# Performance work log

Measured on AMD Instinct MI355X. Metric: run time of the kernel, lower is better.

The kernel has to match this reference:

```python
import jax, jax.numpy as jnp
import numpy as np
from jax import lax

B, N, K = 4, 4096, 64
M1, M2 = 2048, 410  # fps ratios 0.5 then 0.2 (ceil)
EPS = 1e-5  # BatchNorm1d eps


def bn_eval(h, g, be):
    # BatchNorm1d in eval mode with init running stats (mean=0, var=1)
    return h * (g / jnp.sqrt(1.0 + EPS)) + be


def mlp(x, params):
    # Seq(Lin, ReLU, BN) per layer
    for (W, b, g, be) in params:
        x = bn_eval(jax.nn.relu(x @ W + b), g, be)
    return x


def fps(pos, m):
    # farthest point sampling on pos [n,3]; deterministic start at index 0
    n = pos.shape[0]

    def step(carry, _):
        dists, last = carry
        d = jnp.sum((pos - pos[last]) ** 2, axis=-1)
        dists = jnp.minimum(dists, d)
        nxt = jnp.argmax(dists).astype(jnp.int32)
        return (dists, nxt), nxt

    _, rest = lax.scan(step, (jnp.full((n,), jnp.inf, pos.dtype), jnp.int32(0)), None, length=m - 1)
    return jnp.concatenate([jnp.zeros((1,), jnp.int32), rest])


def ball_query(src, q, r):
    # up to K nearest neighbors of each query within radius r
    d2 = jnp.sum((q[:, None, :] - src[None, :, :]) ** 2, axis=-1)  # [M,N]
    negd, idx = lax.top_k(-d2, K)
    return idx, (-negd) <= r * r


def point_conv(x, src_pos, q_pos, idx, mask, params):
    # PyG PointConv: msg = nn(cat[x_j, pos_j - pos_i]); max aggregation
    xj = x[idx]                              # [M,K,C]
    rel = src_pos[idx] - q_pos[:, None, :]   # [M,K,3]
    h = mlp(jnp.concatenate([xj, rel], axis=-1), params)  # [M,K,F]
    h = jnp.where(mask[:, :, None], h, -jnp.inf)
    out = jnp.max(h, axis=1)
    return jnp.where(jnp.any(mask, axis=1)[:, None], out, 0.0)


def sa_module(x, pos, m, radii, params):
    # x [B,n,C], pos [B,n,3]
    idx = jax.vmap(lambda p: fps(p, m))(pos)                       # [B,m]
    q_pos = jnp.take_along_axis(pos, idx[:, :, None], axis=1)      # [B,m,3]
    outs = []
    for r in radii:
        nidx, mask = jax.vmap(lambda s, q: ball_query(s, q, r))(pos, q_pos)
        out = jax.vmap(lambda a, sp, qp, ni, mk: point_conv(a, sp, qp, ni, mk, params))(x, pos, q_pos, nidx, mask)
        outs.append(out)
    return jnp.concatenate(outs, axis=-1), q_pos


def forward(xyz, color, p1, p2, p3, wl1, bl1, wl2, bl2):
    x1, pos1 = sa_module(color, xyz, M1, (0.2, 0.1), p1)     # [B,M1,128]
    x2, pos2 = sa_module(x1, pos1, M2, (0.35, 0.5), p2)      # [B,M2,512]
    h = mlp(jnp.concatenate([x2, pos2], axis=-1), p3)        # [B,M2,1024]
    g = jnp.max(h, axis=1)                                   # global max pool -> [B,1024]
    h1 = jax.nn.relu(g @ wl1 + bl1)                          # dropout inactive (eval)
    out = h1 @ wl2 + bl2
    return out / jnp.linalg.norm(out, axis=1, keepdims=True)


def setup_inputs():
    key = jax.random.key(0)
    ks = jax.random.split(key, 10)

    def w(k, shape):
        return jax.random.normal(k, shape, jnp.float32) * 0.05

    z = lambda n: jnp.zeros((n,), jnp.float32)
    o = lambda n: jnp.ones((n,), jnp.float32)
    return dict(
        xyz=jax.random.uniform(ks[0], (B, N, 3), jnp.float32),
        color=jax.random.uniform(ks[1], (B, N, 3), jnp.float32),
        w1a=w(ks[2], (6, 64)), b1a=z(64), g1a=o(64), be1a=z(64),
        w1b=w(ks[3], (64, 64)), b1b=z(64), g1b=o(64), be1b=z(64),
        w2a=w(ks[4], (131, 128)), b2a=z(128), g2a=o(128), be2a=z(128),
        w2b=w(ks[5], (128, 256)), b2b=z(256), g2b=o(256), be2b=z(256),
        w3=w(ks[6], (515, 1024)), b3=z(1024), g3=o(1024), be3=z(1024),
        wl1=w(ks[7], (1024, 512)), bl1=z(512),
        wl2=w(ks[8], (512, 128)), bl2=z(128),
    )


def reference(xyz, color, w1a, b1a, g1a, be1a, w1b, b1b, g1b, be1b,
              w2a, b2a, g2a, be2a, w2b, b2b, g2b, be2b,
              w3, b3, g3, be3, wl1, bl1, wl2, bl2):
    p1 = [(w1a, b1a, g1a, be1a), (w1b, b1b, g1b, be1b)]
    p2 = [(w2a, b2a, g2a, be2a), (w2b, b2b, g2b, be2b)]
    p3 = [(w3, b3, g3, be3)]
    return forward(xyz, color, p1, p2, p3, wl1, bl1, wl2, bl2)
```

## Files before the change

kernel.cpp:

```cpp
#include <hip/hip_runtime.h>
#include <stdint.h>

#define DEV __device__ __forceinline__

DEV float d2_exact(float ax, float ay, float az, float bx, float by, float bz) {
    float dx = __fsub_rn(ax, bx);
    float dy = __fsub_rn(ay, by);
    float dz = __fsub_rn(az, bz);
    return __fadd_rn(__fadd_rn(__fmul_rn(dx, dx), __fmul_rn(dy, dy)), __fmul_rn(dz, dz));
}

DEV void atomicMaxF(float* a, float v) {
    if (v >= 0.f) atomicMax((int*)a, __float_as_int(v));
    else          atomicMin((unsigned int*)a, __float_as_uint(v));
}

DEV void wave_lds_sync() {
    asm volatile("s_waitcnt lgkmcnt(0)" ::: "memory");
    __builtin_amdgcn_wave_barrier();
}

template<bool MAXRED>
DEV unsigned long long wave_red_u64_l63(unsigned long long k) {
    unsigned lo = (unsigned)k, hi = (unsigned)(k >> 32);
#define DPP_RED_STEP(ctrl, rmask)                                                          \
    {                                                                                      \
        unsigned nlo = (unsigned)__builtin_amdgcn_update_dpp((int)lo, (int)lo, ctrl,       \
                                                             rmask, 0xF, false);           \
        unsigned nhi = (unsigned)__builtin_amdgcn_update_dpp((int)hi, (int)hi, ctrl,       \
                                                             rmask, 0xF, false);           \
        unsigned long long cur = ((unsigned long long)hi << 32) | lo;                      \
        unsigned long long oth = ((unsigned long long)nhi << 32) | nlo;                    \
        bool take = MAXRED ? (oth > cur) : (oth < cur);                                    \
        lo = take ? nlo : lo;                                                              \
        hi = take ? nhi : hi;                                                              \
    }
    DPP_RED_STEP(0x111, 0xF)
    DPP_RED_STEP(0x112, 0xF)
    DPP_RED_STEP(0x114, 0xF)
    DPP_RED_STEP(0x118, 0xF)
    DPP_RED_STEP(0x142, 0xA)
    DPP_RED_STEP(0x143, 0xC)
#undef DPP_RED_STEP
    return ((unsigned long long)hi << 32) | lo;
}

DEV unsigned long long bcast_l63(unsigned long long k) {
    unsigned lo = (unsigned)__builtin_amdgcn_readlane((int)(unsigned)k, 63);
    unsigned hi = (unsigned)__builtin_amdgcn_readlane((int)(unsigned)(k >> 32), 63);
    return ((unsigned long long)hi << 32) | lo;
}

DEV int wave_incl_scan_i32(int v) {
    int t;
    t = __builtin_amdgcn_update_dpp(0, v, 0x111, 0xF, 0xF, true);  v += t;
    t = __builtin_amdgcn_update_dpp(0, v, 0x112, 0xF, 0xF, true);  v += t;
    t = __builtin_amdgcn_update_dpp(0, v, 0x114, 0xF, 0xF, true);  v += t;
    t = __builtin_amdgcn_update_dpp(0, v, 0x118, 0xF, 0xF, true);  v += t;
    t = __builtin_amdgcn_update_dpp(0, v, 0x142, 0xA, 0xF, false); v += t;
    t = __builtin_amdgcn_update_dpp(0, v, 0x143, 0xC, 0xF, false); v += t;
    return v;
}

DEV unsigned wave_min_u32_bcast(unsigned v) {
    int x = (int)v, t;
#define MINSTEP(ctrl, rmask)                                              \
    t = __builtin_amdgcn_update_dpp(-1, x, ctrl, rmask, 0xF, false);      \
    x = ((unsigned)t < (unsigned)x) ? t : x;
    MINSTEP(0x111, 0xF) MINSTEP(0x112, 0xF) MINSTEP(0x114, 0xF)
    MINSTEP(0x118, 0xF) MINSTEP(0x142, 0xA) MINSTEP(0x143, 0xC)
#undef MINSTEP
    return (unsigned)__builtin_amdgcn_readlane(x, 63);
}

DEV void topk64_radix(const float* __restrict__ cD, const int* __restrict__ cI,
                      int cnt, int* buckets, int* nbr, int lane) {
    unsigned prefix = 0;
    int need = 64;
    int shift;
    int done_le_shift = -1;
    for (shift = 24; shift >= 0; shift -= 8) {
        for (int i = lane; i < 256; i += 64) buckets[i] = 0;
        wave_lds_sync();
        for (int e = lane; e < cnt; e += 64) {
            unsigned db = __float_as_uint(cD[e]);
            bool match = (shift == 24) || ((db >> (shift + 8)) == prefix);
            if (match) atomicAdd(&buckets[(db >> shift) & 255], 1);
        }
        wave_lds_sync();
        int c0 = buckets[4 * lane + 0], c1 = buckets[4 * lane + 1];
        int c2 = buckets[4 * lane + 2], c3 = buckets[4 * lane + 3];
        int lsum = c0 + c1 + c2 + c3;
        int excl = wave_incl_scan_i32(lsum) - lsum;
        unsigned packed = 0xFFFFFFFFu;
        int cum = excl;
        int cc[4] = {c0, c1, c2, c3};
#pragma unroll
        for (int j = 0; j < 4; j++) {
            if (cum < need && need <= cum + cc[j])
                packed = ((unsigned)(4 * lane + j) << 20) | (unsigned)cum;
            cum += cc[j];
        }
        unsigned win = wave_min_u32_bcast(packed);
        int B = (int)(win >> 20);
        int bef = (int)(win & 0xFFFFF);
        need -= bef;
        prefix = (shift == 24) ? (unsigned)B : ((prefix << 8) | (unsigned)B);
        int cntB = buckets[B];
        if (cntB == need) { done_le_shift = shift; break; }
    }
    int base = 0;
    if (done_le_shift >= 0) {
        int s = done_le_shift;
        unsigned Pv = prefix;
        for (int e0 = 0; e0 < cnt; e0 += 64) {
            int e = e0 + lane;
            bool sel = false;
            if (e < cnt) sel = ((__float_as_uint(cD[e]) >> s) <= Pv);
            unsigned long long mk = __ballot(sel);
            int pre = __popcll(mk & ((1ull << lane) - 1ull));
            if (sel) nbr[base + pre] = cI[e];
            base += __popcll(mk);
        }
    } else {
        unsigned T = prefix;
        for (int e0 = 0; e0 < cnt; e0 += 64) {
            int e = e0 + lane;
            bool sel = false;
            if (e < cnt) sel = (__float_as_uint(cD[e]) < T);
            unsigned long long mk = __ballot(sel);
            int pre = __popcll(mk & ((1ull << lane) - 1ull));
            if (sel) nbr[base + pre] = cI[e];
            base += __popcll(mk);
        }
        int lastIdx = -1;
        for (int k = 0; k < need; k++) {
            unsigned best = 0xFFFFFFFFu;
            for (int e = lane; e < cnt; e += 64) {
                if (__float_as_uint(cD[e]) == T) {
                    int ix = cI[e];
                    if (ix > lastIdx && (unsigned)ix < best) best = (unsigned)ix;
                }
            }
            best = wave_min_u32_bcast(best);
            if (lane == 0) nbr[base + k] = (int)best;
            lastIdx = (int)best;
        }
    }
}

template<int N, int M, int TPB>
DEV void fps_body(const float* __restrict__ P, float* __restrict__ Q,
                  float* sP, unsigned long long* skey) {
    constexpr int PPT = N / TPB;
    constexpr int NW = TPB / 64;
    const int tid = threadIdx.x;
    const int w = tid >> 6;
    const int lane = tid & 63;

    for (int e = tid; e < N * 3; e += TPB) sP[e] = P[e];
    __syncthreads();

    float px[PPT], py[PPT], pz[PPT], mind[PPT];
#pragma unroll
    for (int p = 0; p < PPT; p++) {
        int i = tid + p * TPB;
        px[p] = sP[3 * i]; py[p] = sP[3 * i + 1]; pz[p] = sP[3 * i + 2];
        mind[p] = __builtin_inff();
    }
    float cx = sP[0], cy = sP[1], cz = sP[2];
    if (tid == 0) { Q[0] = cx; Q[1] = cy; Q[2] = cz; }

    for (int s = 1; s < M; s++) {
        float bestm = -1.f;
        int bidx = 0;
#pragma unroll
        for (int p = 0; p < PPT; p++) {
            float d = d2_exact(px[p], py[p], pz[p], cx, cy, cz);
            float m = fminf(mind[p], d);
            mind[p] = m;
            if (m > bestm) { bestm = m; bidx = tid + p * TPB; }
        }
        unsigned long long key =
            ((unsigned long long)__float_as_uint(bestm) << 32) | (unsigned)(0x7FFFFFFF - bidx);
        key = wave_red_u64_l63<true>(key);
        if (lane == 63) skey[(s & 1) * NW + w] = key;
        __syncthreads();
        const ulonglong2* kv = (const ulonglong2*)(skey + (s & 1) * NW);
        unsigned long long kk = 0ull;
#pragma unroll
        for (int i = 0; i < NW / 2; i++) {
            ulonglong2 v = kv[i];
            unsigned long long m2 = (v.x > v.y) ? v.x : v.y;
            kk = (m2 > kk) ? m2 : kk;
        }
        int sel = 0x7FFFFFFF - (int)(unsigned)(kk & 0xFFFFFFFFu);
        cx = sP[3 * sel]; cy = sP[3 * sel + 1]; cz = sP[3 * sel + 2];
        if (tid == 0) { Q[3 * s] = cx; Q[3 * s + 1] = cy; Q[3 * s + 2] = cz; }
    }
}

__global__ __launch_bounds__(256)
void fps1_kernel(const float* __restrict__ pos, float* __restrict__ qpos) {
    __shared__ float sP[4096 * 3];
    __shared__ __align__(16) unsigned long long skey[2 * 4];
    const int b = blockIdx.x;
    fps_body<4096, 2048, 256>(pos + (size_t)b * 4096 * 3, qpos + (size_t)b * 2048 * 3, sP, skey);
}

#define SA1_CAP 1024

struct Sa1Lds {
    float candD[4][SA1_CAP];
    int   candI[4][SA1_CAP];
    int   nbrS[4][64];
    int   buckets[4][256];
    float vbuf[4][64][8];
    float h1buf[4][64];
};
struct Fps2Lds {
    float sP[2048 * 3];
    unsigned long long skey[2 * 4];
};
union Sa1FusedLds { Sa1Lds sa; Fps2Lds fps; };

__global__ __launch_bounds__(256)
void sa1_fps2_kernel(const float* __restrict__ pos, const float* __restrict__ color,
                     const float* __restrict__ qpos1, float* __restrict__ qpos2,
                     const float* __restrict__ w1, const float* __restrict__ b1,
                     const float* __restrict__ g1, const float* __restrict__ be1,
                     const float* __restrict__ w2, const float* __restrict__ b2,
                     const float* __restrict__ g2, const float* __restrict__ be2,
                     float* __restrict__ x1) {
    __shared__ __align__(16) Sa1FusedLds u;

    if (blockIdx.x < 4) {
        const int b = blockIdx.x;
        fps_body<2048, 410, 256>(qpos1 + (size_t)b * 2048 * 3, qpos2 + (size_t)b * 410 * 3,
                                 u.fps.sP, u.fps.skey);
        return;
    }

    const int lane = threadIdx.x & 63;
    const int w = threadIdx.x >> 6;

    float w1c[6];
#pragma unroll
    for (int i = 0; i < 6; i++) w1c[i] = w1[i * 64 + lane];
    float w2c[64];
#pragma unroll
    for (int i = 0; i < 64; i++) w2c[i] = w2[i * 64 + lane];
    const float rs = rsqrtf(1.0f + 1e-5f);
    const float b1f = b1[lane], s1f = g1[lane] * rs, be1f = be1[lane];
    const float b2f = b2[lane], s2f = g2[lane] * rs, be2f = be2[lane];

    const int gw = (blockIdx.x - 4) * 4 + w;

    for (int it = 0; it < 8; ++it) {
        int p = gw * 8 + it;
        int b = p >> 12;
        int rad = (p >> 11) & 1;
        int q = p & 2047;
        float r2 = (rad == 0) ? (float)(0.2 * 0.2) : (float)(0.1 * 0.1);
        const float* P = pos + (size_t)b * 4096 * 3;
        const float* C = color + (size_t)b * 4096 * 3;
        const float* QP = qpos1 + ((size_t)b * 2048 + q) * 3;
        float qx = QP[0], qy = QP[1], qz = QP[2];

        int cnt = 0;
        for (int c0 = 0; c0 < 4096; c0 += 64) {
            int j = c0 + lane;
            float d2 = d2_exact(P[3 * j], P[3 * j + 1], P[3 * j + 2], qx, qy, qz);
            bool pr = (d2 <= r2);
            unsigned long long mk = __ballot(pr);
            int pre = __popcll(mk & ((1ull << lane) - 1ull));
            int dst = cnt + pre;
            if (pr && dst < SA1_CAP) { u.sa.candD[w][dst] = d2; u.sa.candI[w][dst] = j; }
            cnt += __popcll(mk);
        }
        wave_lds_sync();

        int nV;
        if (cnt <= 64) {
            nV = cnt;
            if (lane < cnt) u.sa.nbrS[w][lane] = u.sa.candI[w][lane];
        } else {
            nV = 64;
            if (cnt <= SA1_CAP) {
                topk64_radix(u.sa.candD[w], u.sa.candI[w], cnt,
                             u.sa.buckets[w], u.sa.nbrS[w], lane);
            } else {
                unsigned long long lastK = 0ull;
                for (int k = 0; k < 64; k++) {
                    unsigned long long bk = ~0ull;
                    for (int j = lane; j < 4096; j += 64) {
                        float d2 = d2_exact(P[3 * j], P[3 * j + 1], P[3 * j + 2], qx, qy, qz);
                        if (d2 <= r2) {
                            unsigned long long ke =
                                ((unsigned long long)__float_as_uint(d2) << 32) | (unsigned)(j + 1);
                            if (ke > lastK && ke < bk) bk = ke;
                        }
                    }
                    bk = wave_red_u64_l63<false>(bk);
                    bk = bcast_l63(bk);
                    if (lane == 0) u.sa.nbrS[w][k] = (int)(unsigned)(bk & 0xFFFFFFFFu) - 1;
                    lastK = bk;
                }
            }
        }
        wave_lds_sync();

        if (lane < nV) {
            int j = u.sa.nbrS[w][lane];
            u.sa.vbuf[w][lane][0] = C[3 * j];
            u.sa.vbuf[w][lane][1] = C[3 * j + 1];
            u.sa.vbuf[w][lane][2] = C[3 * j + 2];
            u.sa.vbuf[w][lane][3] = P[3 * j] - qx;
            u.sa.vbuf[w][lane][4] = P[3 * j + 1] - qy;
            u.sa.vbuf[w][lane][5] = P[3 * j + 2] - qz;
        }
        wave_lds_sync();

        float m = -__builtin_inff();
        for (int n = 0; n < nV; n++) {
            float4 v0 = *reinterpret_cast<const float4*>(&u.sa.vbuf[w][n][0]);
            float4 v1 = *reinterpret_cast<const float4*>(&u.sa.vbuf[w][n][4]);
            float h = b1f;
            h = fmaf(v0.x, w1c[0], h); h = fmaf(v0.y, w1c[1], h); h = fmaf(v0.z, w1c[2], h);
            h = fmaf(v0.w, w1c[3], h); h = fmaf(v1.x, w1c[4], h); h = fmaf(v1.y, w1c[5], h);
            h = fmaxf(h, 0.f);
            h = fmaf(h, s1f, be1f);
            u.sa.h1buf[w][lane] = h;
            wave_lds_sync();
            float a = b2f;
#pragma unroll
            for (int i4 = 0; i4 < 16; i4++) {
                float4 hv = *reinterpret_cast<const float4*>(&u.sa.h1buf[w][i4 * 4]);
                a = fmaf(hv.x, w2c[4 * i4 + 0], a);
                a = fmaf(hv.y, w2c[4 * i4 + 1], a);
                a = fmaf(hv.z, w2c[4 * i4 + 2], a);
                a = fmaf(hv.w, w2c[4 * i4 + 3], a);
            }
            a = fmaxf(a, 0.f);
            a = fmaf(a, s2f, be2f);
            m = fmaxf(m, a);
            __builtin_amdgcn_wave_barrier();
        }
        x1[((size_t)b * 2048 + q) * 128 + rad * 64 + lane] = (nV > 0) ? m : 0.f;
    }
}

struct S2Lds {
    float cD[4][2048];
    int   cI[4][2048];
    int   buckets[4][256];
};
struct YpreLds { float xr[4][4][128]; };
union S2FusedLds { S2Lds s2; YpreLds yp; };

__global__ __launch_bounds__(256)
void sa2sel_ypre_kernel(const float* __restrict__ qpos1, const float* __restrict__ qpos2,
                        int* __restrict__ cntOut, int* __restrict__ nbrOut,
                        const float* __restrict__ x1, const float* __restrict__ w2a,
                        const float* __restrict__ b2a, float* __restrict__ y) {
    __shared__ __align__(16) S2FusedLds u;
    const int lane = threadIdx.x & 63;
    const int w = threadIdx.x >> 6;

    if (blockIdx.x >= 820) {
        int r0 = ((blockIdx.x - 820) * 4 + w) * 4;
#pragma unroll
        for (int rr = 0; rr < 4; rr++) {
            const float* X = x1 + (size_t)(r0 + rr) * 128;
            u.yp.xr[w][rr][lane] = X[lane];
            u.yp.xr[w][rr][lane + 64] = X[lane + 64];
        }
        wave_lds_sync();
        float acc[4][2];
#pragma unroll
        for (int rr = 0; rr < 4; rr++) { acc[rr][0] = b2a[lane]; acc[rr][1] = b2a[lane + 64]; }
        for (int i = 0; i < 128; i++) {
            float w0 = w2a[i * 128 + lane];
            float w1v = w2a[i * 128 + 64 + lane];
#pragma unroll
            for (int rr = 0; rr < 4; rr++) {
                float xv = u.yp.xr[w][rr][i];
                acc[rr][0] = fmaf(xv, w0, acc[rr][0]);
                acc[rr][1] = fmaf(xv, w1v, acc[rr][1]);
            }
        }
#pragma unroll
        for (int rr = 0; rr < 4; rr++) {
            y[(size_t)(r0 + rr) * 128 + lane] = acc[rr][0];
            y[(size_t)(r0 + rr) * 128 + 64 + lane] = acc[rr][1];
        }
        return;
    }

    int p = blockIdx.x * 4 + w;
    int rad = p & 1;
    int q = (p >> 1) % 410;
    int b = (p >> 1) / 410;
    float r2 = (rad == 0) ? (float)(0.35 * 0.35) : 0.25f;
    const float* S = qpos1 + (size_t)b * 2048 * 3;
    const float* QP = qpos2 + ((size_t)b * 410 + q) * 3;
    float qx = QP[0], qy = QP[1], qz = QP[2];

    int cnt = 0;
    for (int c0 = 0; c0 < 2048; c0 += 64) {
        int j = c0 + lane;
        float d2 = d2_exact(S[3 * j], S[3 * j + 1], S[3 * j + 2], qx, qy, qz);
        bool pr = (d2 <= r2);
        unsigned long long mk = __ballot(pr);
        int pre = __popcll(mk & ((1ull << lane) - 1ull));
        if (pr) { u.s2.cD[w][cnt + pre] = d2; u.s2.cI[w][cnt + pre] = j; }
        cnt += __popcll(mk);
    }
    wave_lds_sync();

    int nV = (cnt < 64) ? cnt : 64;
    if (cnt <= 64) {
        if (lane < cnt) nbrOut[(size_t)p * 64 + lane] = u.s2.cI[w][lane];
    } else {
        topk64_radix(u.s2.cD[w], u.s2.cI[w], cnt,
                     u.s2.buckets[w], nbrOut + (size_t)p * 64, lane);
    }
    if (lane == 0) cntOut[p] = nV;
}

__global__ __launch_bounds__(256)
void sa2gemm_kernel(const float* __restrict__ y, const float* __restrict__ qpos1,
                    const float* __restrict__ qpos2, const float* __restrict__ w2a,
                    const float* __restrict__ g2a, const float* __restrict__ be2a,
                    const float* __restrict__ w2b, const float* __restrict__ b2b,
                    const float* __restrict__ g2b, const float* __restrict__ be2b,
                    const int* __restrict__ cntIn, const int* __restrict__ nbrIn,
                    float* __restrict__ A3) {
    __shared__ __align__(16) float h1T[128][68];
    __shared__ __align__(16) float Bs[16][256];
    __shared__ int nbrS[64];

    const int tid = threadIdx.x;
    const int lane = tid & 63;
    const int w = tid >> 6;
    int p = blockIdx.x;
    int rad = p & 1;
    int q = (p >> 1) % 410;
    int b = (p >> 1) / 410;
    int nV = cntIn[p];
    if (tid < 64) nbrS[tid] = nbrIn[(size_t)p * 64 + tid];
    __syncthreads();

    const float* QP = qpos2 + ((size_t)b * 410 + q) * 3;
    float qx = QP[0], qy = QP[1], qz = QP[2];
    const float rs = rsqrtf(1.0f + 1e-5f);
    float wr0a = w2a[128 * 128 + lane], wr1a = w2a[129 * 128 + lane], wr2a = w2a[130 * 128 + lane];
    float wr0b = w2a[128 * 128 + 64 + lane], wr1b = w2a[129 * 128 + 64 + lane], wr2b = w2a[130 * 128 + 64 + lane];
    float sA = g2a[lane] * rs, beA = be2a[lane];
    float sB = g2a[64 + lane] * rs, beB = be2a[64 + lane];

    for (int n = w; n < 64; n += 4) {
        float v0 = 0.f, v1 = 0.f;
        if (n < nV) {
            int j = nbrS[n];
            const float* Y = y + ((size_t)b * 2048 + j) * 128;
            const float* S = qpos1 + ((size_t)b * 2048 + j) * 3;
            float rx = S[0] - qx, ry = S[1] - qy, rz = S[2] - qz;
            float p0 = Y[lane];
            p0 = fmaf(rx, wr0a, p0); p0 = fmaf(ry, wr1a, p0); p0 = fmaf(rz, wr2a, p0);
            float p1 = Y[64 + lane];
            p1 = fmaf(rx, wr0b, p1); p1 = fmaf(ry, wr1b, p1); p1 = fmaf(rz, wr2b, p1);
            v0 = fmaf(fmaxf(p0, 0.f), sA, beA);
            v1 = fmaf(fmaxf(p1, 0.f), sB, beB);
        }
        h1T[lane][n] = v0;
        h1T[64 + lane][n] = v1;
    }
    __syncthreads();

    const int tn = tid & 7;
    const int tf = tid >> 3;
    float acc[8][8];
#pragma unroll
    for (int r = 0; r < 8; r++)
#pragma unroll
        for (int c = 0; c < 8; c++) acc[r][c] = 0.f;

    for (int kt = 0; kt < 8; kt++) {
        __syncthreads();
#pragma unroll
        for (int i = 0; i < 16; i++) {
            int ee = tid + 256 * i;
            int r = ee >> 8, c = ee & 255;
            Bs[r][c] = w2b[(kt * 16 + r) * 256 + c];
        }
        __syncthreads();
#pragma unroll
        for (int kk = 0; kk < 16; kk++) {
            float4 a0 = *reinterpret_cast<const float4*>(&h1T[kt * 16 + kk][tn * 8]);
            float4 a1 = *reinterpret_cast<const float4*>(&h1T[kt * 16 + kk][tn * 8 + 4]);
            float4 b0 = *reinterpret_cast<const float4*>(&Bs[kk][tf * 8]);
            float4 b1 = *reinterpret_cast<const float4*>(&Bs[kk][tf * 8 + 4]);
            float av[8] = {a0.x, a0.y, a0.z, a0.w, a1.x, a1.y, a1.z, a1.w};
            float bv[8] = {b0.x, b0.y, b0.z, b0.w, b1.x, b1.y, b1.z, b1.w};
#pragma unroll
            for (int r = 0; r < 8; r++)
#pragma unroll
                for (int c = 0; c < 8; c++) acc[r][c] = fmaf(av[r], bv[c], acc[r][c]);
        }
    }

    const int f2 = tf * 8;
    float bb[8], ss[8], beb[8];
#pragma unroll
    for (int c = 0; c < 8; c++) {
        bb[c] = b2b[f2 + c];
        ss[c] = g2b[f2 + c] * rs;
        beb[c] = be2b[f2 + c];
    }
    float mx[8];
#pragma unroll
    for (int c = 0; c < 8; c++) mx[c] = -__builtin_inff();
#pragma unroll
    for (int r = 0; r < 8; r++) {
        int n = tn * 8 + r;
        bool val = (n < nV);
#pragma unroll
        for (int c = 0; c < 8; c++) {
            float h = fmaf(fmaxf(acc[r][c] + bb[c], 0.f), ss[c], beb[c]);
            if (val) mx[c] = fmaxf(mx[c], h);
        }
    }
#pragma unroll
    for (int off = 1; off < 8; off <<= 1) {
#pragma unroll
        for (int c = 0; c < 8; c++) {
            float o = __shfl_xor(mx[c], off);
            mx[c] = fmaxf(mx[c], o);
        }
    }
    if (tn == 0) {
        size_t row3 = (size_t)b * 410 + q;
        float* dst = A3 + row3 * 520 + rad * 256 + f2;
#pragma unroll
        for (int c = 0; c < 8; c++) dst[c] = (nV > 0) ? mx[c] : 0.f;
    }
    if (rad == 0 && tid < 3) {
        A3[((size_t)b * 410 + q) * 520 + 512 + tid] = QP[tid];
    }
}

__global__ __launch_bounds__(256)
void l3_kernel(const float* __restrict__ A3, const float* __restrict__ w3,
               const float* __restrict__ b3, const float* __restrict__ g3,
               const float* __restrict__ be3, float* __restrict__ gout) {
    __shared__ float As[32][17];
    __shared__ float Bs[16][256];
    __shared__ float pm[4][256];
    const int tid = threadIdx.x;
    const int rt = blockIdx.x;
    const int ct = blockIdx.y;
    const int b = blockIdx.z;
    const int rgrp = tid >> 6, li = tid & 63;

    float acc[8][4];
#pragma unroll
    for (int r = 0; r < 8; r++)
#pragma unroll
        for (int j = 0; j < 4; j++) acc[r][j] = 0.f;

    for (int kt = 0; kt < 33; kt++) {
        __syncthreads();
        for (int e = tid; e < 512; e += 256) {
            int r = e >> 4, kk = e & 15;
            int row = rt * 32 + r;
            int k = kt * 16 + kk;
            As[r][kk] = (row < 410 && k < 515) ? A3[((size_t)b * 410 + row) * 520 + k] : 0.f;
        }
        for (int e = tid; e < 4096; e += 256) {
            int r = e >> 8, c = e & 255;
            int k = kt * 16 + r;
            Bs[r][c] = (k < 515) ? w3[(size_t)k * 1024 + ct * 256 + c] : 0.f;
        }
        __syncthreads();
#pragma unroll
        for (int kk = 0; kk < 16; kk++) {
            float bvv[4];
#pragma unroll
            for (int j = 0; j < 4; j++) bvv[j] = Bs[kk][li + 64 * j];
#pragma unroll
            for (int r = 0; r < 8; r++) {
                float av = As[rgrp * 8 + r][kk];
#pragma unroll
                for (int j = 0; j < 4; j++) acc[r][j] = fmaf(av, bvv[j], acc[r][j]);
            }
        }
    }

    const float rs = rsqrtf(1.0f + 1e-5f);
    float mx[4], bb[4], ss[4], beb[4];
#pragma unroll
    for (int j = 0; j < 4; j++) {
        int c = ct * 256 + li + 64 * j;
        bb[j] = b3[c]; ss[j] = g3[c] * rs; beb[j] = be3[c];
        mx[j] = -__builtin_inff();
    }
#pragma unroll
    for (int r = 0; r < 8; r++) {
        int row = rt * 32 + rgrp * 8 + r;
        bool val = (row < 410);
#pragma unroll
        for (int j = 0; j < 4; j++) {
            float h = fmaf(fmaxf(acc[r][j] + bb[j], 0.f), ss[j], beb[j]);
            if (val) mx[j] = fmaxf(mx[j], h);
        }
    }
#pragma unroll
    for (int j = 0; j < 4; j++) pm[rgrp][li + 64 * j] = mx[j];
    __syncthreads();
    if (rgrp == 0) {
#pragma unroll
        for (int j = 0; j < 4; j++) {
            int c = li + 64 * j;
            float v = fmaxf(fmaxf(pm[0][c], pm[1][c]), fmaxf(pm[2][c], pm[3][c]));
            atomicMaxF(&gout[b * 1024 + ct * 256 + c], v);
        }
    }
}

__global__ __launch_bounds__(256)
void initg_kernel(float* g) {
    int i = blockIdx.x * 256 + threadIdx.x;
    if (i < 4096) g[i] = -__builtin_inff();
}

__global__ __launch_bounds__(512)
void head_kernel(const float* __restrict__ g, const float* __restrict__ wl1,
                 const float* __restrict__ bl1, const float* __restrict__ wl2,
                 const float* __restrict__ bl2, float* __restrict__ out) {
    __shared__ float gs[1024];
    __shared__ float h1s[512];
    __shared__ float ov[128];
    __shared__ float nrm;
    const int b = blockIdx.x, tid = threadIdx.x;
    gs[tid] = g[b * 1024 + tid];
    gs[tid + 512] = g[b * 1024 + 512 + tid];
    __syncthreads();
    float a = bl1[tid];
#pragma unroll 4
    for (int i = 0; i < 1024; i++) a = fmaf(gs[i], wl1[i * 512 + tid], a);
    h1s[tid] = fmaxf(a, 0.f);
    __syncthreads();
    if (tid < 128) {
        float a2 = bl2[tid];
        for (int i = 0; i < 512; i++) a2 = fmaf(h1s[i], wl2[i * 128 + tid], a2);
        ov[tid] = a2;
    }
    __syncthreads();
    if (tid == 0) {
        float ssum = 0.f;
        for (int i = 0; i < 128; i++) ssum += ov[i] * ov[i];
        nrm = sqrtf(ssum);
    }
    __syncthreads();
    if (tid < 128) out[b * 128 + tid] = ov[tid] / nrm;
}

extern "C" void kernel_launch(void* const* d_in, const int* in_sizes, int n_in,
                              void* d_out, int out_size, void* d_ws, size_t ws_size,
                              hipStream_t stream) {
    const float* xyz   = (const float*)d_in[0];
    const float* color = (const float*)d_in[1];
    const float* w1a = (const float*)d_in[2];
    const float* b1a = (const float*)d_in[3];
    const float* g1a = (const float*)d_in[4];
    const float* be1a = (const float*)d_in[5];
    const float* w1b = (const float*)d_in[6];
    const float* b1b = (const float*)d_in[7];
    const float* g1b = (const float*)d_in[8];
    const float* be1b = (const float*)d_in[9];
    const float* w2a = (const float*)d_in[10];
    const float* b2a = (const float*)d_in[11];
    const float* g2a = (const float*)d_in[12];
    const float* be2a = (const float*)d_in[13];
    const float* w2b = (const float*)d_in[14];
    const float* b2b = (const float*)d_in[15];
    const float* g2b = (const float*)d_in[16];
    const float* be2b = (const float*)d_in[17];
    const float* w3 = (const float*)d_in[18];
    const float* b3 = (const float*)d_in[19];
    const float* g3 = (const float*)d_in[20];
    const float* be3 = (const float*)d_in[21];
    const float* wl1 = (const float*)d_in[22];
    const float* bl1 = (const float*)d_in[23];
    const float* wl2 = (const float*)d_in[24];
    const float* bl2 = (const float*)d_in[25];
    float* out = (float*)d_out;

    float* W = (float*)d_ws;
    float* qpos1 = W;
    float* qpos2 = qpos1 + 24576;
    float* x1    = qpos2 + 4928;
    float* ybuf  = x1 + 1048576;
    float* A3    = ybuf + 1048576;
    float* gbuf  = A3 + 852800;
    int* cntBuf  = (int*)(gbuf + 4096);
    int* nbrBuf  = cntBuf + 3280;

    fps1_kernel<<<4, 256, 0, stream>>>(xyz, qpos1);
    sa1_fps2_kernel<<<516, 256, 0, stream>>>(xyz, color, qpos1, qpos2,
                                             w1a, b1a, g1a, be1a,
                                             w1b, b1b, g1b, be1b, x1);
    sa2sel_ypre_kernel<<<1332, 256, 0, stream>>>(qpos1, qpos2, cntBuf, nbrBuf,
                                                 x1, w2a, b2a, ybuf);
    sa2gemm_kernel<<<3280, 256, 0, stream>>>(ybuf, qpos1, qpos2, w2a, g2a, be2a,
                                             w2b, b2b, g2b, be2b, cntBuf, nbrBuf, A3);
    initg_kernel<<<16, 256, 0, stream>>>(gbuf);
    l3_kernel<<<dim3(13, 4, 4), 256, 0, stream>>>(A3, w3, b3, g3, be3, gbuf);
    head_kernel<<<4, 512, 0, stream>>>(gbuf, wl1, bl1, wl2, bl2, out);
}
```

Baseline: 2.249 ms.

## Overlap FPS1 with SA1 via progress counters and share ball query across radii

```diff
diff --git a/kernel.cpp b/kernel.cpp
--- a/kernel.cpp
+++ b/kernel.cpp
@@ -18,6 +18,14 @@
 DEV void wave_lds_sync() {
     asm volatile("s_waitcnt lgkmcnt(0)" ::: "memory");
     __builtin_amdgcn_wave_barrier();
+}
+
+DEV void wait_prog(int* p, int need) {
+    if ((threadIdx.x & 63) == 0) {
+        while (atomicAdd(p, 0) < need) __builtin_amdgcn_s_sleep(32);
+    }
+    __builtin_amdgcn_wave_barrier();
+    __threadfence();
 }
 
 template<bool MAXRED>
@@ -74,7 +82,7 @@
 }
 
 DEV void topk64_radix(const float* __restrict__ cD, const int* __restrict__ cI,
-                      int cnt, int* buckets, int* nbr, int lane) {
+                      int cnt, float r2lim, int* buckets, int* nbr, int lane) {
     unsigned prefix = 0;
     int need = 64;
     int shift;
@@ -83,7 +91,9 @@
         for (int i = lane; i < 256; i += 64) buckets[i] = 0;
         wave_lds_sync();
         for (int e = lane; e < cnt; e += 64) {
-            unsigned db = __float_as_uint(cD[e]);
+            float dv = cD[e];
+            if (dv > r2lim) continue;
+            unsigned db = __float_as_uint(dv);
             bool match = (shift == 24) || ((db >> (shift + 8)) == prefix);
             if (match) atomicAdd(&buckets[(db >> shift) & 255], 1);
         }
@@ -116,7 +126,7 @@
         for (int e0 = 0; e0 < cnt; e0 += 64) {
             int e = e0 + lane;
             bool sel = false;
-            if (e < cnt) sel = ((__float_as_uint(cD[e]) >> s) <= Pv);
+            if (e < cnt) sel = (cD[e] <= r2lim) && ((__float_as_uint(cD[e]) >> s) <= Pv);
             unsigned long long mk = __ballot(sel);
             int pre = __popcll(mk & ((1ull << lane) - 1ull));
             if (sel) nbr[base + pre] = cI[e];
@@ -127,7 +137,7 @@
         for (int e0 = 0; e0 < cnt; e0 += 64) {
             int e = e0 + lane;
             bool sel = false;
-            if (e < cnt) sel = (__float_as_uint(cD[e]) < T);
+            if (e < cnt) sel = (cD[e] <= r2lim) && (__float_as_uint(cD[e]) < T);
             unsigned long long mk = __ballot(sel);
             int pre = __popcll(mk & ((1ull << lane) - 1ull));
             if (sel) nbr[base + pre] = cI[e];
@@ -137,7 +147,7 @@
         for (int k = 0; k < need; k++) {
             unsigned best = 0xFFFFFFFFu;
             for (int e = lane; e < cnt; e += 64) {
-                if (__float_as_uint(cD[e]) == T) {
+                if (cD[e] <= r2lim && __float_as_uint(cD[e]) == T) {
                     int ix = cI[e];
                     if (ix > lastIdx && (unsigned)ix < best) best = (unsigned)ix;
                 }
@@ -149,9 +159,9 @@
     }
 }
 
-template<int N, int M, int TPB>
+template<int N, int M, int TPB, bool PUB>
 DEV void fps_body(const float* __restrict__ P, float* __restrict__ Q,
-                  float* sP, unsigned long long* skey) {
+                  float* sP, unsigned long long* skey, int* prog) {
     constexpr int PPT = N / TPB;
     constexpr int NW = TPB / 64;
     const int tid = threadIdx.x;
@@ -196,16 +206,14 @@
         }
         int sel = 0x7FFFFFFF - (int)(unsigned)(kk & 0xFFFFFFFFu);
         cx = sP[3 * sel]; cy = sP[3 * sel + 1]; cz = sP[3 * sel + 2];
-        if (tid == 0) { Q[3 * s] = cx; Q[3 * s + 1] = cy; Q[3 * s + 2] = cz; }
-    }
-}
-
-__global__ __launch_bounds__(256)
-void fps1_kernel(const float* __restrict__ pos, float* __restrict__ qpos) {
-    __shared__ float sP[4096 * 3];
-    __shared__ __align__(16) unsigned long long skey[2 * 4];
-    const int b = blockIdx.x;
-    fps_body<4096, 2048, 256>(pos + (size_t)b * 4096 * 3, qpos + (size_t)b * 2048 * 3, sP, skey);
+        if (tid == 0) {
+            Q[3 * s] = cx; Q[3 * s + 1] = cy; Q[3 * s + 2] = cz;
+            if (PUB && ((s + 1) & 63) == 0) {
+                __threadfence();
+                atomicAdd(prog, 64);
+            }
+        }
+    }
 }
 
 #define SA1_CAP 1024
@@ -218,31 +226,31 @@
     float vbuf[4][64][8];
     float h1buf[4][64];
 };
-struct Fps2Lds {
-    float sP[2048 * 3];
+struct Fps1Lds {
+    float sP[4096 * 3];
     unsigned long long skey[2 * 4];
 };
-union Sa1FusedLds { Sa1Lds sa; Fps2Lds fps; };
+union BLds { Sa1Lds sa; Fps1Lds fps; };
 
 __global__ __launch_bounds__(256)
-void sa1_fps2_kernel(const float* __restrict__ pos, const float* __restrict__ color,
-                     const float* __restrict__ qpos1, float* __restrict__ qpos2,
+void fps1_sa1_kernel(const float* __restrict__ pos, const float* __restrict__ color,
+                     float* __restrict__ qpos1,
                      const float* __restrict__ w1, const float* __restrict__ b1,
                      const float* __restrict__ g1, const float* __restrict__ be1,
                      const float* __restrict__ w2, const float* __restrict__ b2,
                      const float* __restrict__ g2, const float* __restrict__ be2,
-                     float* __restrict__ x1) {
-    __shared__ __align__(16) Sa1FusedLds u;
+                     float* __restrict__ x1, int* __restrict__ prog1) {
+    __shared__ __align__(16) BLds u;
+    const int lane = threadIdx.x & 63;
+    const int w = threadIdx.x >> 6;
 
     if (blockIdx.x < 4) {
         const int b = blockIdx.x;
-        fps_body<2048, 410, 256>(qpos1 + (size_t)b * 2048 * 3, qpos2 + (size_t)b * 410 * 3,
-                                 u.fps.sP, u.fps.skey);
+        fps_body<4096, 2048, 256, true>(pos + (size_t)b * 4096 * 3,
+                                        qpos1 + (size_t)b * 2048 * 3,
+                                        u.fps.sP, u.fps.skey, &prog1[b]);
         return;
     }
-
-    const int lane = threadIdx.x & 63;
-    const int w = threadIdx.x >> 6;
 
     float w1c[6];
 #pragma unroll
@@ -250,103 +258,217 @@
     float w2c[64];
 #pragma unroll
     for (int i = 0; i < 64; i++) w2c[i] = w2[i * 64 + lane];
-    const float rs = rsqrtf(1.0f + 1e-5f);
-    const float b1f = b1[lane], s1f = g1[lane] * rs, be1f = be1[lane];
-    const float b2f = b2[lane], s2f = g2[lane] * rs, be2f = be2[lane];
-
-    const int gw = (blockIdx.x - 4) * 4 + w;
-
-    for (int it = 0; it < 8; ++it) {
-        int p = gw * 8 + it;
-        int b = p >> 12;
-        int rad = (p >> 11) & 1;
-        int q = p & 2047;
-        float r2 = (rad == 0) ? (float)(0.2 * 0.2) : (float)(0.1 * 0.1);
-        const float* P = pos + (size_t)b * 4096 * 3;
-        const float* C = color + (size_t)b * 4096 * 3;
-        const float* QP = qpos1 + ((size_t)b * 2048 + q) * 3;
-        float qx = QP[0], qy = QP[1], qz = QP[2];
-
-        int cnt = 0;
+    const float rsc = rsqrtf(1.0f + 1e-5f);
+    const float b1f = b1[lane], s1f = g1[lane] * rsc, be1f = be1[lane];
+    const float b2f = b2[lane], s2f = g2[lane] * rsc, be2f = be2[lane];
+
+    const int sblk = blockIdx.x - 4;
+    const int gw = sblk * 4 + w;
+    const int b = gw >> 9;
+    const int x = gw & 511;
+
+    float* candD_ = u.sa.candD[w];
+    int*   candI_ = u.sa.candI[w];
+    int*   nbrS_  = u.sa.nbrS[w];
+    int*   buckets_ = u.sa.buckets[w];
+    float (*vbuf_)[8] = u.sa.vbuf[w];
+    float* h1buf_ = u.sa.h1buf[w];
+
+    const float r2a = (float)(0.2 * 0.2);
+    const float r2b = (float)(0.1 * 0.1);
+    const float* P = pos + (size_t)b * 4096 * 3;
+    const float* C = color + (size_t)b * 4096 * 3;
+
+#define SA1_MLP(NV, DSTPTR, QX, QY, QZ)                                                   \
+    do {                                                                                  \
+        if (lane < (NV)) {                                                                \
+            int jj = nbrS_[lane];                                                         \
+            vbuf_[lane][0] = C[3 * jj];                                                   \
+            vbuf_[lane][1] = C[3 * jj + 1];                                               \
+            vbuf_[lane][2] = C[3 * jj + 2];                                               \
+            vbuf_[lane][3] = P[3 * jj] - (QX);                                            \
+            vbuf_[lane][4] = P[3 * jj + 1] - (QY);                                        \
+            vbuf_[lane][5] = P[3 * jj + 2] - (QZ);                                        \
+        }                                                                                 \
+        wave_lds_sync();                                                                  \
+        float mmx = -__builtin_inff();                                                    \
+        for (int n = 0; n < (NV); n++) {                                                  \
+            float4 v0 = *reinterpret_cast<const float4*>(&vbuf_[n][0]);                   \
+            float4 v1 = *reinterpret_cast<const float4*>(&vbuf_[n][4]);                   \
+            float h = b1f;                                                                \
+            h = fmaf(v0.x, w1c[0], h); h = fmaf(v0.y, w1c[1], h);                         \
+            h = fmaf(v0.z, w1c[2], h); h = fmaf(v0.w, w1c[3], h);                         \
+            h = fmaf(v1.x, w1c[4], h); h = fmaf(v1.y, w1c[5], h);                         \
+            h = fmaxf(h, 0.f);                                                            \
+            h = fmaf(h, s1f, be1f);                                                       \
+            h1buf_[lane] = h;                                                             \
+            wave_lds_sync();                                                              \
+            float a = b2f;                                                                \
+            _Pragma("unroll")                                                             \
+            for (int i4 = 0; i4 < 16; i4++) {                                             \
+                float4 hv = *reinterpret_cast<const float4*>(&h1buf_[i4 * 4]);            \
+                a = fmaf(hv.x, w2c[4 * i4 + 0], a);                                       \
+                a = fmaf(hv.y, w2c[4 * i4 + 1], a);                                       \
+                a = fmaf(hv.z, w2c[4 * i4 + 2], a);                                       \
+                a = fmaf(hv.w, w2c[4 * i4 + 3], a);                                       \
+            }                                                                             \
+            a = fmaxf(a, 0.f);                                                            \
+            a = fmaf(a, s2f, be2f);                                                       \
+            mmx = fmaxf(mmx, a);                                                          \
+            __builtin_amdgcn_wave_barrier();                                              \
+        }                                                                                 \
+        (DSTPTR)[lane] = ((NV) > 0) ? mmx : 0.f;                                          \
+    } while (0)
+
+    for (int j = 0; j < 4; j++) {
+        int q = j * 512 + x;
+        wait_prog(&prog1[b], q + 1);
+
+        float qx, qy, qz;
+        {
+            int v0 = 0, v1 = 0, v2 = 0;
+            if (lane == 0) {
+                int* qp = (int*)(qpos1 + ((size_t)b * 2048 + q) * 3);
+                v0 = atomicAdd(&qp[0], 0);
+                v1 = atomicAdd(&qp[1], 0);
+                v2 = atomicAdd(&qp[2], 0);
+            }
+            qx = __int_as_float(__shfl(v0, 0));
+            qy = __int_as_float(__shfl(v1, 0));
+            qz = __int_as_float(__shfl(v2, 0));
+        }
+
+        int cnt0 = 0;
         for (int c0 = 0; c0 < 4096; c0 += 64) {
-            int j = c0 + lane;
-            float d2 = d2_exact(P[3 * j], P[3 * j + 1], P[3 * j + 2], qx, qy, qz);
-            bool pr = (d2 <= r2);
+            int jj = c0 + lane;
+            float d2 = d2_exact(P[3 * jj], P[3 * jj + 1], P[3 * jj + 2], qx, qy, qz);
+            bool pr = (d2 <= r2a);
             unsigned long long mk = __ballot(pr);
             int pre = __popcll(mk & ((1ull << lane) - 1ull));
-            int dst = cnt + pre;
-            if (pr && dst < SA1_CAP) { u.sa.candD[w][dst] = d2; u.sa.candI[w][dst] = j; }
-            cnt += __popcll(mk);
+            int dst = cnt0 + pre;
+            if (pr && dst < SA1_CAP) { candD_[dst] = d2; candI_[dst] = jj; }
+            cnt0 += __popcll(mk);
         }
         wave_lds_sync();
 
-        int nV;
-        if (cnt <= 64) {
-            nV = cnt;
-            if (lane < cnt) u.sa.nbrS[w][lane] = u.sa.candI[w][lane];
+        if (cnt0 <= SA1_CAP) {
+            int nV0;
+            if (cnt0 <= 64) {
+                nV0 = cnt0;
+                if (lane < cnt0) nbrS_[lane] = candI_[lane];
+            } else {
+                nV0 = 64;
+                topk64_radix(candD_, candI_, cnt0, __builtin_inff(), buckets_, nbrS_, lane);
+            }
+            wave_lds_sync();
+            SA1_MLP(nV0, &x1[((size_t)b * 2048 + q) * 128 + 0 * 64], qx, qy, qz);
+
+            int cnt1 = 0;
+            for (int e0 = 0; e0 < cnt0; e0 += 64) {
+                int e = e0 + lane;
+                bool pr = (e < cnt0) && (candD_[e] <= r2b);
+                cnt1 += __popcll(__ballot(pr));
+            }
+            int nV1;
+            if (cnt1 <= 64) {
+                nV1 = cnt1;
+                int basec = 0;
+                for (int e0 = 0; e0 < cnt0; e0 += 64) {
+                    int e = e0 + lane;
+                    bool pr = (e < cnt0) && (candD_[e] <= r2b);
+                    unsigned long long mk = __ballot(pr);
+                    int pre = __popcll(mk & ((1ull << lane) - 1ull));
+                    if (pr) nbrS_[basec + pre] = candI_[e];
+                    basec += __popcll(mk);
+                }
+            } else {
+                nV1 = 64;
+                topk64_radix(candD_, candI_, cnt0, r2b, buckets_, nbrS_, lane);
+            }
+            wave_lds_sync();
+            SA1_MLP(nV1, &x1[((size_t)b * 2048 + q) * 128 + 1 * 64], qx, qy, qz);
         } else {
-            nV = 64;
-            if (cnt <= SA1_CAP) {
-                topk64_radix(u.sa.candD[w], u.sa.candI[w], cnt,
-                             u.sa.buckets[w], u.sa.nbrS[w], lane);
-            } else {
+            for (int rad = 0; rad < 2; rad++) {
+                float r2 = (rad == 0) ? r2a : r2b;
+                int cntR = 0;
+                for (int c0 = 0; c0 < 4096; c0 += 64) {
+                    int jj = c0 + lane;
+                    float d2 = d2_exact(P[3 * jj], P[3 * jj + 1], P[3 * jj + 2], qx, qy, qz);
+                    cntR += __popcll(__ballot(d2 <= r2));
+                }
+                int nV = (cntR < 64) ? cntR : 64;
                 unsigned long long lastK = 0ull;
-                for (int k = 0; k < 64; k++) {
+                for (int k = 0; k < nV; k++) {
                     unsigned long long bk = ~0ull;
-                    for (int j = lane; j < 4096; j += 64) {
-                        float d2 = d2_exact(P[3 * j], P[3 * j + 1], P[3 * j + 2], qx, qy, qz);
+                    for (int jj = lane; jj < 4096; jj += 64) {
+                        float d2 = d2_exact(P[3 * jj], P[3 * jj + 1], P[3 * jj + 2], qx, qy, qz);
                         if (d2 <= r2) {
                             unsigned long long ke =
-                                ((unsigned long long)__float_as_uint(d2) << 32) | (unsigned)(j + 1);
+                                ((unsigned long long)__float_as_uint(d2) << 32) | (unsigned)(jj + 1);
                             if (ke > lastK && ke < bk) bk = ke;
                         }
                     }
                     bk = wave_red_u64_l63<false>(bk);
                     bk = bcast_l63(bk);
-                    if (lane == 0) u.sa.nbrS[w][k] = (int)(unsigned)(bk & 0xFFFFFFFFu) - 1;
+                    if (lane == 0) nbrS_[k] = (int)(unsigned)(bk & 0xFFFFFFFFu) - 1;
                     lastK = bk;
                 }
+                wave_lds_sync();
+                SA1_MLP(nV, &x1[((size_t)b * 2048 + q) * 128 + rad * 64], qx, qy, qz);
             }
         }
-        wave_lds_sync();
-
-        if (lane < nV) {
-            int j = u.sa.nbrS[w][lane];
-            u.sa.vbuf[w][lane][0] = C[3 * j];
-            u.sa.vbuf[w][lane][1] = C[3 * j + 1];
-            u.sa.vbuf[w][lane][2] = C[3 * j + 2];
-            u.sa.vbuf[w][lane][3] = P[3 * j] - qx;
-            u.sa.vbuf[w][lane][4] = P[3 * j + 1] - qy;
-            u.sa.vbuf[w][lane][5] = P[3 * j + 2] - qz;
-        }
-        wave_lds_sync();
-
-        float m = -__builtin_inff();
-        for (int n = 0; n < nV; n++) {
-            float4 v0 = *reinterpret_cast<const float4*>(&u.sa.vbuf[w][n][0]);
-            float4 v1 = *reinterpret_cast<const float4*>(&u.sa.vbuf[w][n][4]);
-            float h = b1f;
-            h = fmaf(v0.x, w1c[0], h); h = fmaf(v0.y, w1c[1], h); h = fmaf(v0.z, w1c[2], h);
-            h = fmaf(v0.w, w1c[3], h); h = fmaf(v1.x, w1c[4], h); h = fmaf(v1.y, w1c[5], h);
-            h = fmaxf(h, 0.f);
-            h = fmaf(h, s1f, be1f);
-            u.sa.h1buf[w][lane] = h;
-            wave_lds_sync();
-            float a = b2f;
-#pragma unroll
-            for (int i4 = 0; i4 < 16; i4++) {
-                float4 hv = *reinterpret_cast<const float4*>(&u.sa.h1buf[w][i4 * 4]);
-                a = fmaf(hv.x, w2c[4 * i4 + 0], a);
-                a = fmaf(hv.y, w2c[4 * i4 + 1], a);
-                a = fmaf(hv.z, w2c[4 * i4 + 2], a);
-                a = fmaf(hv.w, w2c[4 * i4 + 3], a);
-            }
-            a = fmaxf(a, 0.f);
-            a = fmaf(a, s2f, be2f);
-            m = fmaxf(m, a);
-            __builtin_amdgcn_wave_barrier();
-        }
-        x1[((size_t)b * 2048 + q) * 128 + rad * 64 + lane] = (nV > 0) ? m : 0.f;
+    }
+#undef SA1_MLP
+}
+
+struct Fps2Lds {
+    float sP[2048 * 3];
+    unsigned long long skey[2 * 4];
+};
+struct YpreLds { float xr[4][4][128]; };
+union CLds { Fps2Lds fps; YpreLds yp; };
+
+__global__ __launch_bounds__(256)
+void fps2_ypre_kernel(const float* __restrict__ qpos1, float* __restrict__ qpos2,
+                      const float* __restrict__ x1, const float* __restrict__ w2a,
+                      const float* __restrict__ b2a, float* __restrict__ y) {
+    __shared__ __align__(16) CLds u;
+    const int lane = threadIdx.x & 63;
+    const int w = threadIdx.x >> 6;
+
+    if (blockIdx.x < 4) {
+        const int b = blockIdx.x;
+        fps_body<2048, 410, 256, false>(qpos1 + (size_t)b * 2048 * 3,
+                                        qpos2 + (size_t)b * 410 * 3,
+                                        u.fps.sP, u.fps.skey, nullptr);
+        return;
+    }
+
+    int r0 = ((blockIdx.x - 4) * 4 + w) * 4;
+#pragma unroll
+    for (int rr = 0; rr < 4; rr++) {
+        const float* X = x1 + (size_t)(r0 + rr) * 128;
+        u.yp.xr[w][rr][lane] = X[lane];
+        u.yp.xr[w][rr][lane + 64] = X[lane + 64];
+    }
+    wave_lds_sync();
+    float acc[4][2];
+#pragma unroll
+    for (int rr = 0; rr < 4; rr++) { acc[rr][0] = b2a[lane]; acc[rr][1] = b2a[lane + 64]; }
+    for (int i = 0; i < 128; i++) {
+        float w0 = w2a[i * 128 + lane];
+        float w1v = w2a[i * 128 + 64 + lane];
+#pragma unroll
+        for (int rr = 0; rr < 4; rr++) {
+            float xv = u.yp.xr[w][rr][i];
+            acc[rr][0] = fmaf(xv, w0, acc[rr][0]);
+            acc[rr][1] = fmaf(xv, w1v, acc[rr][1]);
+        }
+    }
+#pragma unroll
+    for (int rr = 0; rr < 4; rr++) {
+        y[(size_t)(r0 + rr) * 128 + lane] = acc[rr][0];
+        y[(size_t)(r0 + rr) * 128 + 64 + lane] = acc[rr][1];
     }
 }
 
@@ -355,48 +477,13 @@
     int   cI[4][2048];
     int   buckets[4][256];
 };
-struct YpreLds { float xr[4][4][128]; };
-union S2FusedLds { S2Lds s2; YpreLds yp; };
 
 __global__ __launch_bounds__(256)
-void sa2sel_ypre_kernel(const float* __restrict__ qpos1, const float* __restrict__ qpos2,
-                        int* __restrict__ cntOut, int* __restrict__ nbrOut,
-                        const float* __restrict__ x1, const float* __restrict__ w2a,
-                        const float* __restrict__ b2a, float* __restrict__ y) {
-    __shared__ __align__(16) S2FusedLds u;
+void sa2sel_kernel(const float* __restrict__ qpos1, const float* __restrict__ qpos2,
+                   int* __restrict__ cntOut, int* __restrict__ nbrOut) {
+    __shared__ __align__(16) S2Lds u;
     const int lane = threadIdx.x & 63;
     const int w = threadIdx.x >> 6;
-
-    if (blockIdx.x >= 820) {
-        int r0 = ((blockIdx.x - 820) * 4 + w) * 4;
-#pragma unroll
-        for (int rr = 0; rr < 4; rr++) {
-            const float* X = x1 + (size_t)(r0 + rr) * 128;
-            u.yp.xr[w][rr][lane] = X[lane];
-            u.yp.xr[w][rr][lane + 64] = X[lane + 64];
-        }
-        wave_lds_sync();
-        float acc[4][2];
-#pragma unroll
-        for (int rr = 0; rr < 4; rr++) { acc[rr][0] = b2a[lane]; acc[rr][1] = b2a[lane + 64]; }
-        for (int i = 0; i < 128; i++) {
-            float w0 = w2a[i * 128 + lane];
-            float w1v = w2a[i * 128 + 64 + lane];
-#pragma unroll
-            for (int rr = 0; rr < 4; rr++) {
-                float xv = u.yp.xr[w][rr][i];
-                acc[rr][0] = fmaf(xv, w0, acc[rr][0]);
-                acc[rr][1] = fmaf(xv, w1v, acc[rr][1]);
-            }
-        }
-#pragma unroll
-        for (int rr = 0; rr < 4; rr++) {
-            y[(size_t)(r0 + rr) * 128 + lane] = acc[rr][0];
-            y[(size_t)(r0 + rr) * 128 + 64 + lane] = acc[rr][1];
-        }
-        return;
-    }
-
     int p = blockIdx.x * 4 + w;
     int rad = p & 1;
     int q = (p >> 1) % 410;
@@ -413,17 +500,17 @@
         bool pr = (d2 <= r2);
         unsigned long long mk = __ballot(pr);
         int pre = __popcll(mk & ((1ull << lane) - 1ull));
-        if (pr) { u.s2.cD[w][cnt + pre] = d2; u.s2.cI[w][cnt + pre] = j; }
+        if (pr) { u.cD[w][cnt + pre] = d2; u.cI[w][cnt + pre] = j; }
         cnt += __popcll(mk);
     }
     wave_lds_sync();
 
     int nV = (cnt < 64) ? cnt : 64;
     if (cnt <= 64) {
-        if (lane < cnt) nbrOut[(size_t)p * 64 + lane] = u.s2.cI[w][lane];
+        if (lane < cnt) nbrOut[(size_t)p * 64 + lane] = u.cI[w][lane];
     } else {
-        topk64_radix(u.s2.cD[w], u.s2.cI[w], cnt,
-                     u.s2.buckets[w], nbrOut + (size_t)p * 64, lane);
+        topk64_radix(u.cD[w], u.cI[w], cnt, __builtin_inff(),
+                     u.buckets[w], nbrOut + (size_t)p * 64, lane);
     }
     if (lane == 0) cntOut[p] = nV;
 }
@@ -629,9 +716,10 @@
 }
 
 __global__ __launch_bounds__(256)
-void initg_kernel(float* g) {
+void init_kernel(float* g, int* prog1) {
     int i = blockIdx.x * 256 + threadIdx.x;
     if (i < 4096) g[i] = -__builtin_inff();
+    if (i < 4) prog1[i] = 0;
 }
 
 __global__ __launch_bounds__(512)
@@ -706,16 +794,16 @@
     float* gbuf  = A3 + 852800;
     int* cntBuf  = (int*)(gbuf + 4096);
     int* nbrBuf  = cntBuf + 3280;
-
-    fps1_kernel<<<4, 256, 0, stream>>>(xyz, qpos1);
-    sa1_fps2_kernel<<<516, 256, 0, stream>>>(xyz, color, qpos1, qpos2,
+    int* prog1   = nbrBuf + 209920;
+
+    init_kernel<<<16, 256, 0, stream>>>(gbuf, prog1);
+    fps1_sa1_kernel<<<516, 256, 0, stream>>>(xyz, color, qpos1,
                                              w1a, b1a, g1a, be1a,
-                                             w1b, b1b, g1b, be1b, x1);
-    sa2sel_ypre_kernel<<<1332, 256, 0, stream>>>(qpos1, qpos2, cntBuf, nbrBuf,
-                                                 x1, w2a, b2a, ybuf);
+                                             w1b, b1b, g1b, be1b, x1, prog1);
+    fps2_ypre_kernel<<<516, 256, 0, stream>>>(qpos1, qpos2, x1, w2a, b2a, ybuf);
+    sa2sel_kernel<<<820, 256, 0, stream>>>(qpos1, qpos2, cntBuf, nbrBuf);
     sa2gemm_kernel<<<3280, 256, 0, stream>>>(ybuf, qpos1, qpos2, w2a, g2a, be2a,
                                              w2b, b2b, g2b, be2b, cntBuf, nbrBuf, A3);
-    initg_kernel<<<16, 256, 0, stream>>>(gbuf);
     l3_kernel<<<dim3(13, 4, 4), 256, 0, stream>>>(A3, w3, b3, g3, be3, gbuf);
     head_kernel<<<4, 512, 0, stream>>>(gbuf, wl1, bl1, wl2, bl2, out);
 }
```

After: 2.081 ms. 1.08x faster.
